# Kernel optimization log

Hardware: AMD Instinct MI355X
Metric: run time of the kernel (lower is better)

Reference implementation:

```python
import jax, jax.numpy as jnp
import numpy as np

BN_EPS = 1e-5
L2_EPS = 1e-12

def _conv2d(x, w, pad):
    # x: NCHW, w: OIHW
    return jax.lax.conv_general_dilated(
        x, w, window_strides=(1, 1), padding=[(pad, pad), (pad, pad)],
        dimension_numbers=('NCHW', 'OIHW', 'NCHW'))

def _l2norm(x, axis):
    n = jnp.sqrt(jnp.sum(x * x, axis=axis, keepdims=True))
    return x / jnp.maximum(n, L2_EPS)

def setup_inputs() -> dict:
    key = jax.random.key(0)
    ks = jax.random.split(key, 8)
    x = jax.random.normal(ks[0], (16, 512, 32, 32), dtype=jnp.float32)
    w_proj1 = jax.random.normal(ks[1], (512, 512, 3, 3), dtype=jnp.float32) * 0.02
    bn_gamma = jnp.ones((512,), dtype=jnp.float32)
    bn_beta = jnp.zeros((512,), dtype=jnp.float32)
    bn_mean = jnp.zeros((512,), dtype=jnp.float32)
    bn_var = jnp.ones((512,), dtype=jnp.float32)
    w_proj2 = jax.random.normal(ks[2], (512, 512, 3, 3), dtype=jnp.float32) * 0.02
    w_assign = jax.random.normal(ks[3], (64, 512, 1, 1), dtype=jnp.float32)
    centroids = jax.random.uniform(ks[4], (64, 512), dtype=jnp.float32)
    return {'x': x, 'w_proj1': w_proj1, 'bn_gamma': bn_gamma, 'bn_beta': bn_beta,
            'bn_mean': bn_mean, 'bn_var': bn_var, 'w_proj2': w_proj2,
            'w_assign': w_assign, 'centroids': centroids}

def reference(x, w_proj1, bn_gamma, bn_beta, bn_mean, bn_var, w_proj2, w_assign, centroids):
    # projection head: conv3x3 -> BN (eval) -> ReLU -> conv3x3
    h = _conv2d(x, w_proj1, pad=1)
    inv = jax.lax.rsqrt(bn_var + BN_EPS)
    h = (h - bn_mean[None, :, None, None]) * (bn_gamma * inv)[None, :, None, None] + bn_beta[None, :, None, None]
    h = jax.nn.relu(h)
    x_enc = _conv2d(h, w_proj2, pad=1)

    # descriptor-wise L2 normalization over channels
    xn = _l2norm(x_enc, axis=1)
    N, C, H, W = xn.shape
    K = w_assign.shape[0]

    # soft assignment: 1x1 conv -> softmax over clusters
    sa = _conv2d(xn, w_assign, pad=0).reshape(N, K, H * W)  # [N,K,L]
    sa = jax.nn.softmax(sa, axis=1)

    xf = xn.reshape(N, C, H * W)  # [N,C,L]
    # algebraic rewrite of the per-cluster residual loop:
    # vlad[n,k,c] = sum_l sa[n,k,l]*(xf[n,c,l] - cent[k,c])
    vlad = jnp.einsum('nkl,ncl->nkc', sa, xf) - sa.sum(-1)[:, :, None] * centroids[None]
    vlad = _l2norm(vlad, axis=2)          # intra-normalization
    vlad = vlad.reshape(N, K * C)
    vlad = _l2norm(vlad, axis=1)          # global L2 norm
    return (vlad, x_enc)
```

## Files before the change

### kernel.cpp

```cpp
#include <hip/hip_runtime.h>
#include <math.h>


typedef __bf16 bf16x8 __attribute__((ext_vector_type(8)));
typedef float f32x4 __attribute__((ext_vector_type(4)));

#define GLDS16(gp, lp)                                                  \
  __builtin_amdgcn_global_load_lds(                                     \
      (const __attribute__((address_space(1))) void*)(gp),              \
      (__attribute__((address_space(3))) void*)(lp), 16, 0, 0)

template <int MODE>
__global__ __launch_bounds__(256) void conv_gemm(
    const __bf16* __restrict__ in,
    const __bf16* __restrict__ wt,
    const float* __restrict__ scale, const float* __restrict__ shift,
    __bf16* __restrict__ outp) {
  __shared__ __align__(16) __bf16 Hl[6 * 42 * 64];
  __shared__ __align__(16) __bf16 Wl[128 * 64];

  const int t = threadIdx.x;
  const int bx = blockIdx.x, oT = blockIdx.y;
  const int lane = t & 63, wid = t >> 6;
  const int l16 = lane & 15, q = lane >> 4;
  const int wrow = wid >> 1, wcol = wid & 1;

  const int n = bx >> 3;
  const int trow0 = (bx & 7) * 4;

  const int swr = t >> 3, sp = t & 7;
  const __bf16* wsrc[4];
#pragma unroll
  for (int i = 0; i < 4; ++i)
    wsrc[i] = wt + (size_t)(oT * 128 + 32 * i + swr) * 4608 + sp * 8;

  const __bf16* inb = in + (size_t)n * (1156 * 512);
  const __bf16* hsrc[8];
  bool hval[8];
#pragma unroll
  for (int i = 0; i < 8; ++i) {
    const int jj = t + 256 * i;
    hval[i] = jj < 2016;
    const int hr = jj / 336;
    const int hrem = jj - hr * 336;
    const int hw = hrem >> 3, hc8 = hrem & 7;
    hsrc[i] = inb + ((size_t)((trow0 + hr) * 34 + hw)) * 512 +
              (hc8 ^ (hw & 7)) * 8;
  }

  const int c0 = (q ^ (l16 & 7)) * 8;
  const int c1 = ((4 + q) ^ (l16 & 7)) * 8;
  int aoff[4], prow_[4], pcol_[4];
#pragma unroll
  for (int i = 0; i < 4; ++i) {
    aoff[i] = (wrow * 64 + i * 16 + l16) * 64;
    const int p = wcol * 64 + i * 16 + l16;
    prow_[i] = p >> 5;
    pcol_[i] = p & 31;
  }

  f32x4 acc[4][4];
#pragma unroll
  for (int i = 0; i < 4; ++i)
#pragma unroll
    for (int j = 0; j < 4; ++j) acc[i][j] = (f32x4){0.f, 0.f, 0.f, 0.f};

#pragma unroll 1
  for (int cc = 0; cc < 8; ++cc) {
#pragma unroll
    for (int i = 0; i < 8; ++i)
      if (hval[i]) GLDS16(hsrc[i] + cc * 64, Hl + (t + 256 * i) * 8);
#pragma unroll 1
    for (int tap = 0; tap < 9; ++tap) {
      const int woffs = (tap * 8 + cc) * 64;
#pragma unroll
      for (int i = 0; i < 4; ++i)
        GLDS16(wsrc[i] + woffs, Wl + (t + 256 * i) * 8);
      __syncthreads();

      const int dh = tap / 3, dw = tap - dh * 3;
      bf16x8 aw[4][2], bp[4][2];
#pragma unroll
      for (int i = 0; i < 4; ++i) {
        aw[i][0] = *(const bf16x8*)&Wl[aoff[i] + c0];
        aw[i][1] = *(const bf16x8*)&Wl[aoff[i] + c1];
      }
#pragma unroll
      for (int i = 0; i < 4; ++i) {
        const int col = pcol_[i] + dw;
        const int rb = (prow_[i] + dh) * 2688 + col * 64;
        const int xr = col & 7;
        bp[i][0] = *(const bf16x8*)&Hl[rb + (q ^ xr) * 8];
        bp[i][1] = *(const bf16x8*)&Hl[rb + ((4 + q) ^ xr) * 8];
      }
#pragma unroll
      for (int kh = 0; kh < 2; ++kh)
#pragma unroll
        for (int mt = 0; mt < 4; ++mt)
#pragma unroll
          for (int nt = 0; nt < 4; ++nt)
            acc[mt][nt] = __builtin_amdgcn_mfma_f32_16x16x32_bf16(
                aw[mt][kh], bp[nt][kh], acc[mt][nt], 0, 0, 0);
      __syncthreads();
    }
  }

#pragma unroll
  for (int nt = 0; nt < 4; ++nt) {
    const int m_l = wcol * 64 + nt * 16 + l16;
    const int mg2 = bx * 128 + m_l;
    const int n2 = mg2 >> 10, pix2 = mg2 & 1023;
#pragma unroll
    for (int mt = 0; mt < 4; ++mt) {
      const int ob = oT * 128 + wrow * 64 + mt * 16 + q * 4;
      f32x4 v = acc[mt][nt];
      union {
        __bf16 b[4];
        uint2 u;
      } pk;
      if (MODE == 0) {
        const f32x4 sc = *(const f32x4*)&scale[ob];
        const f32x4 sh = *(const f32x4*)&shift[ob];
#pragma unroll
        for (int r = 0; r < 4; ++r)
          pk.b[r] = (__bf16)fmaxf(v[r] * sc[r] + sh[r], 0.f);
        __bf16* dst = outp +
                      ((size_t)n2 * 1156 + ((pix2 >> 5) + 1) * 34 +
                       ((pix2 & 31) + 1)) * 512 + ob;
        *(uint2*)dst = pk.u;
      } else {
#pragma unroll
        for (int r = 0; r < 4; ++r) pk.b[r] = (__bf16)v[r];
        __bf16* dst = outp + ((size_t)n2 * 1024 + pix2) * 512 + ob;
        *(uint2*)dst = pk.u;
      }
    }
  }
}

__global__ __launch_bounds__(256) void xform(const float* __restrict__ x,
                                             __bf16* __restrict__ xpad) {
  const int n = blockIdx.x >> 5, h = blockIdx.x & 31;
  const int t = threadIdx.x;
  const int w = t & 31, cg = t >> 5;
  const float* src = x + ((size_t)n * 512 + cg * 64) * 1024 + h * 32 + w;
  __bf16* dst =
      xpad + ((size_t)n * 1156 + (h + 1) * 34 + (w + 1)) * 512 + cg * 64;
  union {
    __bf16 b[8];
    uint4 u;
  } pk;
#pragma unroll 1
  for (int jj = 0; jj < 8; ++jj) {
#pragma unroll
    for (int j = 0; j < 8; ++j) pk.b[j] = (__bf16)src[(jj * 8 + j) * 1024];
    *(uint4*)(dst + jj * 8) = pk.u;
  }
}

__global__ __launch_bounds__(256) void expand_x(const __bf16* __restrict__ xebT,
                                                float* __restrict__ xenc,
                                                __bf16* __restrict__ xeb) {
  __shared__ __align__(16) __bf16 Ll[64 * 64];
  const int t = threadIdx.x;
  const int cc = blockIdx.x, ptile = blockIdx.y, n = blockIdx.z;
  const int p0 = ptile * 64, c0 = cc * 64;
#pragma unroll
  for (int i = 0; i < 2; ++i) {
    const int u = t * 2 + i;
    const int pix = u >> 3, c8 = u & 7;
    uint4 v =
        *(const uint4*)&xebT[((size_t)n * 1024 + p0 + pix) * 512 + c0 + c8 * 8];
    *(uint4*)&Ll[pix * 64 + (c8 ^ (pix & 7)) * 8] = v;
  }
  __syncthreads();
  const int c = t >> 2, g = t & 3;
  union {
    float f[4];
    float4 v;
  } fv[4];
  union {
    __bf16 b[16];
    uint4 u[2];
  } bv;
#pragma unroll
  for (int r = 0; r < 16; ++r) {
    const int pix = g * 16 + r;
    __bf16 b = Ll[pix * 64 + ((c >> 3) ^ (pix & 7)) * 8 + (c & 7)];
    bv.b[r] = b;
    fv[r >> 2].f[r & 3] = (float)b;
  }
  float* fd = xenc + ((size_t)n * 512 + c0 + c) * 1024 + p0 + g * 16;
#pragma unroll
  for (int r = 0; r < 4; ++r) *(float4*)(fd + r * 4) = fv[r].v;
  __bf16* bd = xeb + ((size_t)n * 512 + c0 + c) * 1024 + p0 + g * 16;
  *(uint4*)bd = bv.u[0];
  *(uint4*)(bd + 8) = bv.u[1];
}

__global__ __launch_bounds__(256) void assign_softmax(
    const __bf16* __restrict__ xebT, const __bf16* __restrict__ watb,
    __bf16* __restrict__ saPb, float* __restrict__ S) {
  __shared__ __align__(16) __bf16 Al[64 * 32];
  __shared__ __align__(16) __bf16 Wlb[64 * 32];
  __shared__ float Sl[64];
  const int t = threadIdx.x;
  const int pt = blockIdx.x, n = blockIdx.y;
  const int lane = t & 63, wid = t >> 6;
  const int l16 = lane & 15, q = lane >> 4;
  if (t < 64) Sl[t] = 0.f;

  const int arow = t >> 2;
  const __bf16* asrc = xebT + ((size_t)n * 1024 + pt * 64 + arow) * 512 +
                       ((t & 3) ^ ((arow >> 1) & 3)) * 8;
  const __bf16* wsrc = watb + (size_t)(t >> 2) * 512 + (t & 3) * 8;
  const int ldsb = wid * 512;
  const int sw = (q ^ ((l16 >> 1) & 3)) * 8;
  const int pnoff = (t >> 2) * 32 + (t & 3) * 8;

  f32x4 acc[4];
#pragma unroll
  for (int i = 0; i < 4; ++i) acc[i] = (f32x4){0.f, 0.f, 0.f, 0.f};
  float pn = 0.f;

#pragma unroll 1
  for (int kc = 0; kc < 16; ++kc) {
    GLDS16(asrc + kc * 32, Al + ldsb);
    GLDS16(wsrc + kc * 32, Wlb + ldsb);
    __syncthreads();
    {
      bf16x8 v = *(const bf16x8*)&Al[pnoff];
#pragma unroll
      for (int j = 0; j < 8; ++j) {
        float f = (float)v[j];
        pn = fmaf(f, f, pn);
      }
    }
    bf16x8 pf = *(const bf16x8*)&Al[(wid * 16 + l16) * 32 + sw];
    bf16x8 wf[4];
#pragma unroll
    for (int ka = 0; ka < 4; ++ka)
      wf[ka] = *(const bf16x8*)&Wlb[(ka * 16 + l16) * 32 + sw];
#pragma unroll
    for (int ka = 0; ka < 4; ++ka)
      acc[ka] =
          __builtin_amdgcn_mfma_f32_16x16x32_bf16(wf[ka], pf, acc[ka], 0, 0, 0);
    __syncthreads();
  }
  pn += __shfl_xor(pn, 1);
  pn += __shfl_xor(pn, 2);
  const float rn = 1.0f / fmaxf(sqrtf(__shfl(pn, l16 * 4)), 1e-12f);

  float sc[16];
  float m = -3.4e38f;
#pragma unroll
  for (int ka = 0; ka < 4; ++ka)
#pragma unroll
    for (int r = 0; r < 4; ++r) {
      float v = acc[ka][r] * rn;
      sc[ka * 4 + r] = v;
      m = fmaxf(m, v);
    }
  m = fmaxf(m, __shfl_xor(m, 16));
  m = fmaxf(m, __shfl_xor(m, 32));
  float s = 0.f;
#pragma unroll
  for (int j = 0; j < 16; ++j) {
    sc[j] = __expf(sc[j] - m);
    s += sc[j];
  }
  s += __shfl_xor(s, 16);
  s += __shfl_xor(s, 32);
  const float inv = 1.0f / s;
  const int pixg = pt * 64 + wid * 16 + l16;
#pragma unroll
  for (int j = 0; j < 16; ++j) {
    const int k = (j >> 2) * 16 + q * 4 + (j & 3);
    float sa = sc[j] * inv;
    sc[j] = sa;
    saPb[((size_t)n * 64 + k) * 1024 + pixg] = (__bf16)(sa * rn);
  }
#pragma unroll
  for (int j = 0; j < 16; ++j) {
    float v = sc[j];
    v += __shfl_xor(v, 1);
    v += __shfl_xor(v, 2);
    v += __shfl_xor(v, 4);
    v += __shfl_xor(v, 8);
    sc[j] = v;
  }
  if (l16 == 0) {
#pragma unroll
    for (int j = 0; j < 16; ++j)
      atomicAdd(&Sl[(j >> 2) * 16 + q * 4 + (j & 3)], sc[j]);
  }
  __syncthreads();
  if (t < 64) atomicAdd(&S[n * 64 + t], Sl[t]);
}

__global__ __launch_bounds__(256) void vlad_gemm(
    const __bf16* __restrict__ saPb, const __bf16* __restrict__ xeb,
    float* __restrict__ vpart) {
  __shared__ __align__(16) __bf16 Al[64 * 32];
  __shared__ __align__(16) __bf16 Bl[128 * 32];

  const int t = threadIdx.x;
  const int cT = blockIdx.x, n = blockIdx.y, ks = blockIdx.z;
  const int lane = t & 63, wid = t >> 6;
  const int l16 = lane & 15, q = lane >> 4;
  const int wrow = wid >> 1, wcol = wid & 1;

  const int ar = t >> 2, acp = t & 3;
  const __bf16* asrc = saPb + (size_t)n * 65536 + (size_t)ar * 1024 + ks * 256 +
                       (acp ^ ((ar >> 1) & 3)) * 8;
  const int br0 = t >> 2, bcp0 = t & 3;
  const int br1 = (t + 256) >> 2, bcp1 = t & 3;
  const __bf16* bsrc0 = xeb + (size_t)n * 524288 +
                        (size_t)(cT * 128 + br0) * 1024 + ks * 256 +
                        (bcp0 ^ ((br0 >> 1) & 3)) * 8;
  const __bf16* bsrc1 = xeb + (size_t)n * 524288 +
                        (size_t)(cT * 128 + br1) * 1024 + ks * 256 +
                        (bcp1 ^ ((br1 >> 1) & 3)) * 8;

  const int ldsb = wid * 512;
  const int sw = (q ^ ((l16 >> 1) & 3)) * 8;

  f32x4 acc[2][4];
#pragma unroll
  for (int i = 0; i < 2; ++i)
#pragma unroll
    for (int j = 0; j < 4; ++j) acc[i][j] = (f32x4){0.f, 0.f, 0.f, 0.f};

#pragma unroll 1
  for (int kc = 0; kc < 8; ++kc) {
    GLDS16(asrc + kc * 32, Al + ldsb);
    GLDS16(bsrc0 + kc * 32, Bl + ldsb);
    GLDS16(bsrc1 + kc * 32, Bl + 2048 + ldsb);
    __syncthreads();

    bf16x8 af[2], bf[4];
#pragma unroll
    for (int i = 0; i < 2; ++i)
      af[i] = *(const bf16x8*)&Al[(wrow * 32 + i * 16 + l16) * 32 + sw];
#pragma unroll
    for (int i = 0; i < 4; ++i)
      bf[i] = *(const bf16x8*)&Bl[(wcol * 64 + i * 16 + l16) * 32 + sw];
#pragma unroll
    for (int mt = 0; mt < 2; ++mt)
#pragma unroll
      for (int nt = 0; nt < 4; ++nt)
        acc[mt][nt] = __builtin_amdgcn_mfma_f32_16x16x32_bf16(
            af[mt], bf[nt], acc[mt][nt], 0, 0, 0);
    __syncthreads();
  }

  float* vp = vpart + (size_t)(ks * 16 + n) * 32768;
#pragma unroll
  for (int mt = 0; mt < 2; ++mt) {
    const int krow = wrow * 32 + mt * 16 + q * 4;
#pragma unroll
    for (int nt = 0; nt < 4; ++nt) {
      const int ccol = cT * 128 + wcol * 64 + nt * 16 + l16;
#pragma unroll
      for (int r = 0; r < 4; ++r)
        vp[(size_t)(krow + r) * 512 + ccol] = acc[mt][nt][r];
    }
  }
}

__global__ __launch_bounds__(64) void intra_norm(float* __restrict__ vraw,
                                                 const float* __restrict__ vpart,
                                                 const float* __restrict__ S,
                                                 const float* __restrict__ cent,
                                                 float* __restrict__ gss) {
  const int b = blockIdx.x;
  const int n = b >> 6, k = b & 63;
  const int lane = threadIdx.x;
  const float s = S[b];
  float v[8];
  float ss = 0.f;
#pragma unroll
  for (int j = 0; j < 8; ++j) {
    const int c = lane * 8 + j;
    const size_t off = (size_t)b * 512 + c;
    float val = vpart[off] + vpart[524288 + off] + vpart[2 * 524288 + off] +
                vpart[3 * 524288 + off] - s * cent[k * 512 + c];
    v[j] = val;
    ss += val * val;
  }
#pragma unroll
  for (int off = 1; off < 64; off <<= 1) ss += __shfl_xor(ss, off);
  const float rn = 1.0f / fmaxf(sqrtf(ss), 1e-12f);
#pragma unroll
  for (int j = 0; j < 8; ++j) vraw[(size_t)b * 512 + lane * 8 + j] = v[j] * rn;
  if (lane == 0) atomicAdd(&gss[n], ss * rn * rn);
}

__global__ __launch_bounds__(256) void finalize(const float* __restrict__ vraw,
                                                const float* __restrict__ gss,
                                                float* __restrict__ out) {
  const int id = blockIdx.x * 256 + threadIdx.x;
  const int n = id >> 15;
  out[id] = vraw[id] * (1.0f / fmaxf(sqrtf(gss[n]), 1e-12f));
}

__global__ __launch_bounds__(256) void zero_border(__bf16* __restrict__ xpad,
                                                   __bf16* __restrict__ hpad) {
  const int id = blockIdx.x * 256 + threadIdx.x;
  const int n = id / 8448;
  const int rem = id - n * 8448;
  const int pb = rem >> 6;
  const int c8 = rem & 63;
  int h, w;
  if (pb < 34) {
    h = 0;
    w = pb;
  } else if (pb < 68) {
    h = 33;
    w = pb - 34;
  } else {
    const int r2 = pb - 68;
    h = 1 + (r2 >> 1);
    w = (r2 & 1) * 33;
  }
  __bf16* base = blockIdx.y ? hpad : xpad;
  *(uint4*)(base + ((size_t)n * 1156 + h * 34 + w) * 512 + c8 * 8) =
      (uint4){0u, 0u, 0u, 0u};
}

__global__ __launch_bounds__(256) void wt_prep(const float* __restrict__ w1,
                                               const float* __restrict__ w2,
                                               __bf16* __restrict__ wt1,
                                               __bf16* __restrict__ wt2) {
  __shared__ float Lw[4608];
  const int o = blockIdx.x;
  const float* w = blockIdx.y ? w2 : w1;
  __bf16* wt = blockIdx.y ? wt2 : wt1;
  const int t = threadIdx.x;
#pragma unroll
  for (int i = 0; i < 18; ++i)
    Lw[t + 256 * i] = w[(size_t)o * 4608 + t + 256 * i];
  __syncthreads();
#pragma unroll
  for (int i = 0; i < 18; ++i) {
    const int idk = t + 256 * i;
    const int kt = idk >> 6;
    const int p = (idk >> 3) & 7, e = idk & 7;
    const int logical = p ^ (o & 7);
    const int k2 = kt * 64 + logical * 8 + e;
    const int tap = k2 >> 9, ci = k2 & 511;
    wt[(size_t)o * 4608 + idk] = (__bf16)Lw[ci * 9 + tap];
  }
}

__global__ void misc_prep(const float* g, const float* b, const float* m,
                          const float* v, const float* wA, float* scale,
                          float* shift, __bf16* watb, float* Sz) {
  const int i = blockIdx.x * 256 + threadIdx.x;
  if (i < 512) {
    float sc = g[i] / sqrtf(v[i] + 1e-5f);
    scale[i] = sc;
    shift[i] = b[i] - m[i] * sc;
  } else if (i < 512 + 32768) {
    const int id = i - 512;
    const int k = id >> 9, j = id & 511;
    const int kt = j >> 5, cpos = (j >> 3) & 3, e = j & 7;
    const int c = kt * 32 + (cpos ^ ((k >> 1) & 3)) * 8 + e;
    watb[(size_t)k * 512 + j] = (__bf16)wA[(size_t)k * 512 + c];
  } else if (i < 512 + 32768 + 1040) {
    Sz[i - (512 + 32768)] = 0.f;
  }
}

extern "C" void kernel_launch(void* const* d_in, const int* in_sizes, int n_in,
                              void* d_out, int out_size, void* d_ws,
                              size_t ws_size, hipStream_t stream) {
  const float* x = (const float*)d_in[0];
  const float* w1 = (const float*)d_in[1];
  const float* gam = (const float*)d_in[2];
  const float* bet = (const float*)d_in[3];
  const float* mean = (const float*)d_in[4];
  const float* var = (const float*)d_in[5];
  const float* w2 = (const float*)d_in[6];
  const float* wA = (const float*)d_in[7];
  const float* cent = (const float*)d_in[8];
  float* out = (float*)d_out;

  char* ws = (char*)d_ws;
  __bf16* Wt1 = (__bf16*)(ws + 0);
  __bf16* Wt2 = (__bf16*)(ws + 4718592);
  __bf16* xpad = (__bf16*)(ws + 9437184);
  __bf16* xebT = (__bf16*)(ws + 9437184);
  __bf16* saPb = (__bf16*)(ws + 26214400);
  __bf16* hpad = (__bf16*)(ws + 28377088);
  __bf16* xeb = (__bf16*)(ws + 28377088);
  float* vpart = (float*)(ws + 0);
  float* vraw = (float*)(ws + 8388608);
  float* scale = (float*)(ws + 47316992);
  float* shift = (float*)(ws + 47319040);
  __bf16* watb = (__bf16*)(ws + 47321088);
  float* S = (float*)(ws + 47386624);
  float* gss = (float*)(ws + 47390720);

  float* xenc = out + 524288;

  zero_border<<<dim3(528, 2), 256, 0, stream>>>(xpad, hpad);
  misc_prep<<<135, 256, 0, stream>>>(gam, bet, mean, var, wA, scale, shift,
                                     watb, S);
  wt_prep<<<dim3(512, 2), 256, 0, stream>>>(w1, w2, Wt1, Wt2);
  xform<<<512, 256, 0, stream>>>(x, xpad);

  conv_gemm<0><<<dim3(128, 4), 256, 0, stream>>>(xpad, Wt1, scale, shift, hpad);
  conv_gemm<1><<<dim3(128, 4), 256, 0, stream>>>(hpad, Wt2, nullptr, nullptr,
                                                 xebT);

  expand_x<<<dim3(8, 16, 16), 256, 0, stream>>>(xebT, xenc, xeb);
  assign_softmax<<<dim3(16, 16), 256, 0, stream>>>(xebT, watb, saPb, S);
  vlad_gemm<<<dim3(4, 16, 4), 256, 0, stream>>>(saPb, xeb, vpart);
  intra_norm<<<1024, 64, 0, stream>>>(vraw, vpart, S, cent, gss);
  finalize<<<2048, 256, 0, stream>>>(vraw, gss, out);
}
```

Measured before the change: 321.4 us.

## Double-buffer conv weight tiles in LDS and flatten loop into prefetched pipeline

Merges the channel-chunk and tap loops into one 72-step loop and double-buffers the weight tile in LDS. The tile for step s+2 is issued right after the fragments for step s have been read into registers, and the input halo for the next channel chunk is fetched the same way. Explicit vmcnt/lgkmcnt waits and raw barriers replace the two __syncthreads per step, so global-to-LDS loads can overlap the MFMA work. It also raises wave priority around the MFMA block, at the cost of doubling the weight LDS footprint and relying on hand-counted wait values.

New measurement: 316.0 us. Within noise of the previous version (-1.7%).

```diff
diff --git a/kernel.cpp b/kernel.cpp
--- a/kernel.cpp
+++ b/kernel.cpp
@@ -17,7 +17,7 @@
     const float* __restrict__ scale, const float* __restrict__ shift,
     __bf16* __restrict__ outp) {
   __shared__ __align__(16) __bf16 Hl[6 * 42 * 64];
-  __shared__ __align__(16) __bf16 Wl[128 * 64];
+  __shared__ __align__(16) __bf16 Wl[2 * 128 * 64];
 
   const int t = threadIdx.x;
   const int bx = blockIdx.x, oT = blockIdx.y;
@@ -65,43 +65,88 @@
 #pragma unroll
     for (int j = 0; j < 4; ++j) acc[i][j] = (f32x4){0.f, 0.f, 0.f, 0.f};
 
+#pragma unroll
+  for (int i = 0; i < 8; ++i)
+    if (hval[i]) GLDS16(hsrc[i], Hl + (t + 256 * i) * 8);
+#pragma unroll
+  for (int i = 0; i < 4; ++i)
+    GLDS16(wsrc[i], Wl + (t + 256 * i) * 8);
+#pragma unroll
+  for (int i = 0; i < 4; ++i)
+    GLDS16(wsrc[i] + 512, Wl + 8192 + (t + 256 * i) * 8);
+  asm volatile("s_waitcnt vmcnt(4)" ::: "memory");
+  __builtin_amdgcn_s_barrier();
+
+  int tap = 0, dh = 0, dw = 0, cc = 0;
+  int tap2 = 2, cc2 = 0;
+
 #pragma unroll 1
-  for (int cc = 0; cc < 8; ++cc) {
-#pragma unroll
-    for (int i = 0; i < 8; ++i)
-      if (hval[i]) GLDS16(hsrc[i] + cc * 64, Hl + (t + 256 * i) * 8);
-#pragma unroll 1
-    for (int tap = 0; tap < 9; ++tap) {
-      const int woffs = (tap * 8 + cc) * 64;
+  for (int s = 0; s < 72; ++s) {
+    const int buf = (s & 1) << 13;
+    const __bf16* Wb = Wl + buf;
+
+    bf16x8 aw[4][2], bp[4][2];
+#pragma unroll
+    for (int i = 0; i < 4; ++i) {
+      aw[i][0] = *(const bf16x8*)&Wb[aoff[i] + c0];
+      aw[i][1] = *(const bf16x8*)&Wb[aoff[i] + c1];
+    }
+#pragma unroll
+    for (int i = 0; i < 4; ++i) {
+      const int col = pcol_[i] + dw;
+      const int rb = (prow_[i] + dh) * 2688 + col * 64;
+      const int xr = col & 7;
+      bp[i][0] = *(const bf16x8*)&Hl[rb + (q ^ xr) * 8];
+      bp[i][1] = *(const bf16x8*)&Hl[rb + ((4 + q) ^ xr) * 8];
+    }
+    asm volatile("s_waitcnt lgkmcnt(0)" ::: "memory");
+    __builtin_amdgcn_sched_barrier(0);
+    __builtin_amdgcn_s_barrier();
+
+    if (tap == 8 && cc < 7) {
+#pragma unroll
+      for (int i = 0; i < 8; ++i)
+        if (hval[i]) GLDS16(hsrc[i] + (cc + 1) * 64, Hl + (t + 256 * i) * 8);
+    }
+    if (s < 70) {
+      const int woffs2 = (tap2 * 8 + cc2) * 64;
 #pragma unroll
       for (int i = 0; i < 4; ++i)
-        GLDS16(wsrc[i] + woffs, Wl + (t + 256 * i) * 8);
-      __syncthreads();
-
-      const int dh = tap / 3, dw = tap - dh * 3;
-      bf16x8 aw[4][2], bp[4][2];
-#pragma unroll
-      for (int i = 0; i < 4; ++i) {
-        aw[i][0] = *(const bf16x8*)&Wl[aoff[i] + c0];
-        aw[i][1] = *(const bf16x8*)&Wl[aoff[i] + c1];
-      }
-#pragma unroll
-      for (int i = 0; i < 4; ++i) {
-        const int col = pcol_[i] + dw;
-        const int rb = (prow_[i] + dh) * 2688 + col * 64;
-        const int xr = col & 7;
-        bp[i][0] = *(const bf16x8*)&Hl[rb + (q ^ xr) * 8];
-        bp[i][1] = *(const bf16x8*)&Hl[rb + ((4 + q) ^ xr) * 8];
-      }
-#pragma unroll
-      for (int kh = 0; kh < 2; ++kh)
-#pragma unroll
-        for (int mt = 0; mt < 4; ++mt)
-#pragma unroll
-          for (int nt = 0; nt < 4; ++nt)
-            acc[mt][nt] = __builtin_amdgcn_mfma_f32_16x16x32_bf16(
-                aw[mt][kh], bp[nt][kh], acc[mt][nt], 0, 0, 0);
-      __syncthreads();
+        GLDS16(wsrc[i] + woffs2, Wl + buf + (t + 256 * i) * 8);
+    }
+
+    __builtin_amdgcn_s_setprio(1);
+#pragma unroll
+    for (int kh = 0; kh < 2; ++kh)
+#pragma unroll
+      for (int mt = 0; mt < 4; ++mt)
+#pragma unroll
+        for (int nt = 0; nt < 4; ++nt)
+          acc[mt][nt] = __builtin_amdgcn_mfma_f32_16x16x32_bf16(
+              aw[mt][kh], bp[nt][kh], acc[mt][nt], 0, 0, 0);
+    __builtin_amdgcn_s_setprio(0);
+
+    if (s < 70)
+      asm volatile("s_waitcnt vmcnt(4)" ::: "memory");
+    else
+      asm volatile("s_waitcnt vmcnt(0)" ::: "memory");
+    __builtin_amdgcn_s_barrier();
+
+    ++tap;
+    ++dw;
+    if (dw == 3) {
+      dw = 0;
+      ++dh;
+    }
+    if (tap == 9) {
+      tap = 0;
+      dh = 0;
+      dw = 0;
+      ++cc;
+    }
+    if (++tap2 == 9) {
+      tap2 = 0;
+      ++cc2;
     }
   }
 
```
